# Kernel tuning notes

Hardware: AMD Instinct MI355X
Metric: run time of the kernel (lower is better)

The kernel has to match this reference:

```python
import jax, jax.numpy as jnp
import numpy as np
from jax import lax

D_MODEL = 512
D_STATE = 16
D_CONV = 4
EXPAND = 2
D_INNER = EXPAND * D_MODEL
DT_RANK = (D_MODEL + 15) // 16  # 32


def _mamba_dir(x, in_w, conv_w, conv_b, xproj_w, dt_w, dt_b, A_log, D, out_w):
    # x: (B, L, d_model)
    B, L, _ = x.shape
    xz = jnp.einsum('bld,ed->ble', x, in_w)          # (B, L, 2*d_inner)
    xi, z = jnp.split(xz, 2, axis=-1)                # each (B, L, d_inner)
    # causal depthwise conv over time
    xc = xi.transpose(0, 2, 1)                       # (B, d_inner, L)
    xc = lax.conv_general_dilated(
        xc, conv_w, window_strides=(1,), padding=[(D_CONV - 1, 0)],
        feature_group_count=D_INNER, dimension_numbers=('NCH', 'OIH', 'NCH'))
    xi = jax.nn.silu(xc + conv_b[None, :, None]).transpose(0, 2, 1)  # (B, L, d_inner)
    # input-dependent SSM params
    x_dbl = jnp.einsum('bld,ed->ble', xi, xproj_w)   # (B, L, dt_rank + 2*d_state)
    dt, Bc, Cc = jnp.split(x_dbl, [DT_RANK, DT_RANK + D_STATE], axis=-1)
    delta = jax.nn.softplus(jnp.einsum('blr,dr->bld', dt, dt_w) + dt_b)  # (B, L, d_inner)
    A = -jnp.exp(A_log)                              # (d_inner, d_state)
    deltaA = jnp.exp(delta[..., None] * A)           # (B, L, d_inner, d_state)
    dBx = delta[..., None] * Bc[:, :, None, :] * xi[..., None]  # (B, L, d_inner, d_state)

    def step(h, inputs):
        dA_t, dBx_t, C_t = inputs
        h = dA_t * h + dBx_t                         # (B, d_inner, d_state)
        y = jnp.einsum('bdn,bn->bd', h, C_t)
        return h, y

    h0 = jnp.zeros((B, D_INNER, D_STATE), dtype=x.dtype)
    _, ys = lax.scan(step, h0,
                     (deltaA.transpose(1, 0, 2, 3),
                      dBx.transpose(1, 0, 2, 3),
                      Cc.transpose(1, 0, 2)))
    y = ys.transpose(1, 0, 2)                        # (B, L, d_inner)
    y = y + xi * D
    y = y * jax.nn.silu(z)
    return jnp.einsum('ble,de->bld', y, out_w)       # (B, L, d_model)


def _forward(x, f_in_w, f_conv_w, f_conv_b, f_xproj_w, f_dt_w, f_dt_b, f_A_log, f_D, f_out_w,
             b_in_w, b_conv_w, b_conv_b, b_xproj_w, b_dt_w, b_dt_b, b_A_log, b_D, b_out_w,
             fusion_w, fusion_b, ln_g, ln_b):
    out_fwd = _mamba_dir(x, f_in_w, f_conv_w, f_conv_b, f_xproj_w, f_dt_w, f_dt_b, f_A_log, f_D, f_out_w)
    x_flip = jnp.flip(x, axis=1)
    out_bwd = _mamba_dir(x_flip, b_in_w, b_conv_w, b_conv_b, b_xproj_w, b_dt_w, b_dt_b, b_A_log, b_D, b_out_w)
    out_bwd = jnp.flip(out_bwd, axis=1)
    fused = jnp.concatenate([out_fwd, out_bwd], axis=-1)     # (B, L, 2*d_model)
    out = jnp.einsum('blf,df->bld', fused, fusion_w) + fusion_b
    r = x + out
    mu = jnp.mean(r, axis=-1, keepdims=True)
    var = jnp.var(r, axis=-1, keepdims=True)
    return (r - mu) * lax.rsqrt(var + 1e-5) * ln_g + ln_b


def _mamba_params(key):
    ks = jax.random.split(key, 6)
    s = 0.02
    in_w = jax.random.normal(ks[0], (2 * D_INNER, D_MODEL), jnp.float32) * s
    conv_w = jax.random.normal(ks[1], (D_INNER, 1, D_CONV), jnp.float32) * 0.2
    conv_b = jnp.zeros((D_INNER,), jnp.float32)
    xproj_w = jax.random.normal(ks[2], (DT_RANK + 2 * D_STATE, D_INNER), jnp.float32) * s
    dt_w = jax.random.normal(ks[3], (D_INNER, DT_RANK), jnp.float32) * (DT_RANK ** -0.5)
    dt_b = jax.random.uniform(ks[4], (D_INNER,), jnp.float32, -4.0, -2.0)
    A_log = jnp.log(jnp.broadcast_to(jnp.arange(1, D_STATE + 1, dtype=jnp.float32), (D_INNER, D_STATE)))
    D = jnp.ones((D_INNER,), jnp.float32)
    out_w = jax.random.normal(ks[5], (D_MODEL, D_INNER), jnp.float32) * s
    return in_w, conv_w, conv_b, xproj_w, dt_w, dt_b, A_log, D, out_w


def setup_inputs() -> dict:
    key = jax.random.key(0)
    kx, kf, kb, k1, k2 = jax.random.split(key, 5)
    B, L = 2, 1024
    x = jax.random.normal(kx, (B, L, D_MODEL), jnp.float32)
    f = _mamba_params(kf)
    b = _mamba_params(kb)
    fusion_w = jax.random.normal(k1, (D_MODEL, 2 * D_MODEL), jnp.float32) * 0.02
    fusion_b = jnp.zeros((D_MODEL,), jnp.float32)
    ln_g = jnp.ones((D_MODEL,), jnp.float32)
    ln_b = jnp.zeros((D_MODEL,), jnp.float32)
    names_f = ['f_in_w', 'f_conv_w', 'f_conv_b', 'f_xproj_w', 'f_dt_w', 'f_dt_b', 'f_A_log', 'f_D', 'f_out_w']
    names_b = ['b_in_w', 'b_conv_w', 'b_conv_b', 'b_xproj_w', 'b_dt_w', 'b_dt_b', 'b_A_log', 'b_D', 'b_out_w']
    d = {'x': x, 'fusion_w': fusion_w, 'fusion_b': fusion_b, 'ln_g': ln_g, 'ln_b': ln_b}
    d.update(dict(zip(names_f, f)))
    d.update(dict(zip(names_b, b)))
    return d


def reference(x, f_in_w, f_conv_w, f_conv_b, f_xproj_w, f_dt_w, f_dt_b, f_A_log, f_D, f_out_w,
              b_in_w, b_conv_w, b_conv_b, b_xproj_w, b_dt_w, b_dt_b, b_A_log, b_D, b_out_w,
              fusion_w, fusion_b, ln_g, ln_b):
    return _forward(x, f_in_w, f_conv_w, f_conv_b, f_xproj_w, f_dt_w, f_dt_b, f_A_log, f_D, f_out_w,
                    b_in_w, b_conv_w, b_conv_b, b_xproj_w, b_dt_w, b_dt_b, b_A_log, b_D, b_out_w,
                    fusion_w, fusion_b, ln_g, ln_b)
```

## Files before the change

kernel.cpp:

```cpp
#include <hip/hip_runtime.h>
#include <hip/hip_bf16.h>

typedef __bf16 bf16x8 __attribute__((ext_vector_type(8)));
typedef __bf16 bf16x4 __attribute__((ext_vector_type(4)));
typedef float  f32x4  __attribute__((ext_vector_type(4)));

#define LOG2E 1.44269504088896340f

static __device__ __forceinline__ unsigned short f2bf_bits(float f) {
  unsigned u = __builtin_bit_cast(unsigned, f);
  u = u + 0x7FFFu + ((u >> 16) & 1u);
  return (unsigned short)(u >> 16);
}
static __device__ __forceinline__ __bf16 to_bf16(float f) {
  unsigned short s = f2bf_bits(f);
  return __builtin_bit_cast(__bf16, s);
}
static __device__ __forceinline__ float fast_sigmoid(float x) {
  return __builtin_amdgcn_rcpf(1.f + __builtin_amdgcn_exp2f(-LOG2E * x));
}
static __device__ __forceinline__ float softplus_f(float x) {
  float m = fmaxf(x, 0.f);
  float e = __builtin_amdgcn_exp2f(-LOG2E * fabsf(x));
  return fmaf(__builtin_amdgcn_logf(1.f + e), 1.f / LOG2E, m);
}

struct CastSeg { const float* src; __bf16* dst; int n4; };
struct CastArgs { CastSeg s[8]; };

__global__ __launch_bounds__(256) void cast_kernel(CastArgs a) {
  CastSeg seg = a.s[blockIdx.y];
  int idx = blockIdx.x * 256 + threadIdx.x;
  int stride = gridDim.x * 256;
  const float4* src = (const float4*)seg.src;
  bf16x4* dst = (bf16x4*)seg.dst;
  for (int i = idx; i < seg.n4; i += stride) {
    float4 v = src[i];
    bf16x4 o;
    o[0] = to_bf16(v.x); o[1] = to_bf16(v.y);
    o[2] = to_bf16(v.z); o[3] = to_bf16(v.w);
    dst[i] = o;
  }
}

template<typename OutT, bool BIAS, bool RESID, bool SPLIT>
__global__ __launch_bounds__(256) void gemm_bt(
    const __bf16* __restrict__ A, long long sAz,
    const __bf16* __restrict__ B0, const __bf16* __restrict__ B1,
    OutT* __restrict__ C, long long sCz, int ldc,
    int N, int K,
    const float* __restrict__ bias, const float* __restrict__ resid, int ldr,
    float* __restrict__ xiout, __bf16* __restrict__ gateout, long long sXz)
{
  const __bf16* B = (blockIdx.z == 0) ? B0 : B1;
  A += (size_t)blockIdx.z * (size_t)sAz;
  C += (size_t)blockIdx.z * (size_t)sCz;
  if (SPLIT) {
    xiout  += (size_t)blockIdx.z * (size_t)sXz;
    gateout += (size_t)blockIdx.z * (size_t)sXz;
  }
  int lane = threadIdx.x & 63;
  int wid  = threadIdx.x >> 6;
  int rowBase = blockIdx.y * 128 + (wid >> 1) * 64;
  int colBase = blockIdx.x * 128 + (wid & 1) * 64;
  int lr = lane & 15;
  int lk = (lane >> 4) << 3;
  const __bf16* Ap = A + (size_t)(rowBase + lr) * K + lk;
  const __bf16* Bp[4];
  #pragma unroll
  for (int ni = 0; ni < 4; ++ni) {
    int br = colBase + ni * 16 + lr;
    if (br > N - 1) br = N - 1;
    Bp[ni] = B + (size_t)br * K + lk;
  }
  f32x4 acc[4][4] = {};
  #pragma unroll 2
  for (int k = 0; k < K; k += 32) {
    bf16x8 aF[4], bF[4];
    #pragma unroll
    for (int mi = 0; mi < 4; ++mi)
      aF[mi] = *(const bf16x8*)(Ap + (size_t)(mi * 16) * K + k);
    #pragma unroll
    for (int ni = 0; ni < 4; ++ni)
      bF[ni] = *(const bf16x8*)(Bp[ni] + k);
    #pragma unroll
    for (int mi = 0; mi < 4; ++mi)
      #pragma unroll
      for (int ni = 0; ni < 4; ++ni)
        acc[mi][ni] = __builtin_amdgcn_mfma_f32_16x16x32_bf16(aF[mi], bF[ni], acc[mi][ni], 0, 0, 0);
  }
  int crow = rowBase + ((lane >> 4) << 2);
  int ccol = colBase + lr;
  #pragma unroll
  for (int mi = 0; mi < 4; ++mi) {
    #pragma unroll
    for (int ni = 0; ni < 4; ++ni) {
      int c = ccol + ni * 16;
      if (c < N) {
        #pragma unroll
        for (int j = 0; j < 4; ++j) {
          int r = crow + mi * 16 + j;
          float v = acc[mi][ni][j];
          if (SPLIT) {
            if (c < 1024) xiout[(size_t)r * 1024 + c] = v;
            else          gateout[(size_t)r * 1024 + (c - 1024)] =
                              to_bf16(v * fast_sigmoid(v));
          } else {
            if (BIAS)  v += bias[c];
            if (RESID) v += resid[(size_t)r * ldr + c];
            if constexpr (sizeof(OutT) == 2) C[(size_t)r * ldc + c] = to_bf16(v);
            else                             C[(size_t)r * ldc + c] = v;
          }
        }
      }
    }
  }
}

#define CT 16
__global__ __launch_bounds__(256) void conv_silu_kernel(
    const float* __restrict__ xiraw,
    const float* __restrict__ f_cw, const float* __restrict__ f_cb,
    const float* __restrict__ b_cw, const float* __restrict__ b_cb,
    float* __restrict__ xi32,
    __bf16* __restrict__ xi16)
{
  int d  = blockIdx.x * 256 + threadIdx.x;
  int t0 = blockIdx.y * CT;
  int dir = blockIdx.z >> 1, b = blockIdx.z & 1;
  const float* cw = dir ? b_cw : f_cw;
  const float* cb = dir ? b_cb : f_cb;
  float w0 = cw[d*4+0], w1 = cw[d*4+1], w2 = cw[d*4+2], w3 = cw[d*4+3];
  float bias = cb[d];
  size_t rowBase = (size_t)dir * 2048 + (size_t)b * 1024;
  const float* xp = xiraw + rowBase * 1024 + d;
  float* o32 = xi32 + rowBase * 1024 + d;
  __bf16* o16 = xi16 + rowBase * 1024 + d;
  float xv[CT + 3];
  if (dir == 0) {
    #pragma unroll
    for (int j = 0; j < CT + 3; ++j) {
      int t = t0 - 3 + j;
      xv[j] = (t >= 0) ? xp[(size_t)t * 1024] : 0.f;
    }
    #pragma unroll
    for (int j = 0; j < CT; ++j) {
      int t = t0 + j;
      float v = fmaf(w0, xv[j], fmaf(w1, xv[j+1], fmaf(w2, xv[j+2], fmaf(w3, xv[j+3], bias))));
      float s = v * fast_sigmoid(v);
      o32[(size_t)t * 1024] = s;
      o16[(size_t)t * 1024] = to_bf16(s);
    }
  } else {
    #pragma unroll
    for (int j = 0; j < CT + 3; ++j) {
      int t = t0 + j;
      xv[j] = (t < 1024) ? xp[(size_t)t * 1024] : 0.f;
    }
    #pragma unroll
    for (int j = 0; j < CT; ++j) {
      int t = t0 + j;
      float v = fmaf(w3, xv[j], fmaf(w2, xv[j+1], fmaf(w1, xv[j+2], fmaf(w0, xv[j+3], bias))));
      float s = v * fast_sigmoid(v);
      o32[(size_t)t * 1024] = s;
      o16[(size_t)t * 1024] = to_bf16(s);
    }
  }
}

__global__ __launch_bounds__(256) void g2_kernel(
    const __bf16* __restrict__ A,
    const __bf16* __restrict__ B0, const __bf16* __restrict__ B1,
    float* __restrict__ partial)
{
  int slice = blockIdx.x;
  int mt = blockIdx.y;
  int dir = blockIdx.z;
  const __bf16* B = dir ? B1 : B0;
  const __bf16* Ad = A + (size_t)dir * 2048 * 1024;
  int lane = threadIdx.x & 63, wid = threadIdx.x >> 6;
  int rowBase = mt * 64 + wid * 16;
  int lr = lane & 15, lk = (lane >> 4) << 3;
  int k0 = slice * 256;
  const __bf16* Ap = Ad + (size_t)(rowBase + lr) * 1024 + k0 + lk;
  const __bf16* Bp[4];
  #pragma unroll
  for (int ni = 0; ni < 4; ++ni)
    Bp[ni] = B + (size_t)(ni * 16 + lr) * 1024 + k0 + lk;
  f32x4 acc[4] = {};
  #pragma unroll
  for (int k = 0; k < 256; k += 32) {
    bf16x8 aF = *(const bf16x8*)(Ap + k);
    #pragma unroll
    for (int ni = 0; ni < 4; ++ni) {
      bf16x8 bF = *(const bf16x8*)(Bp[ni] + k);
      acc[ni] = __builtin_amdgcn_mfma_f32_16x16x32_bf16(aF, bF, acc[ni], 0, 0, 0);
    }
  }
  int crow = rowBase + ((lane >> 4) << 2);
  float* out = partial + ((size_t)dir * 4 + slice) * 2048 * 64;
  #pragma unroll
  for (int ni = 0; ni < 4; ++ni)
    #pragma unroll
    for (int j = 0; j < 4; ++j)
      out[(size_t)(crow + j) * 64 + ni * 16 + lr] = acc[ni][j];
}

__global__ __launch_bounds__(256) void g2red_kernel(
    const float4* __restrict__ partial, float4* __restrict__ xdbl)
{
  int idx = blockIdx.x * 256 + threadIdx.x;
  int dir = idx >> 15;
  int rest = idx & 32767;
  const float4* p = partial + (size_t)dir * 4 * 32768 + rest;
  float4 a = p[0], b = p[32768], c = p[2 * 32768], d = p[3 * 32768];
  float4 s;
  s.x = a.x + b.x + c.x + d.x;
  s.y = a.y + b.y + c.y + d.y;
  s.z = a.z + b.z + c.z + d.z;
  s.w = a.w + b.w + c.w + d.w;
  xdbl[idx] = s;
}

#define NC 64
#define CL 16

__global__ __launch_bounds__(256) void scan_part1(
    const float* __restrict__ xi32,
    const float* __restrict__ xdbl,
    const float* __restrict__ f_dtw, const float* __restrict__ f_dtb,
    const float* __restrict__ b_dtw, const float* __restrict__ b_dtb,
    const float* __restrict__ f_Alog, const float* __restrict__ b_Alog,
    float4* __restrict__ aProd, float4* __restrict__ hPart)
{
  int d = blockIdx.x * 256 + threadIdx.x;
  int g = blockIdx.y;
  int zb = blockIdx.z;
  int dir = zb >> 1, b = zb & 1;
  const float* dtw = (dir ? b_dtw : f_dtw) + d * 32;
  float w[32];
  #pragma unroll
  for (int k = 0; k < 32; ++k) w[k] = dtw[k];
  float dtb = (dir ? b_dtb : f_dtb)[d];
  const float* Alog = (dir ? b_Alog : f_Alog) + d * 16;
  float As[16];
  #pragma unroll
  for (int n = 0; n < 16; ++n)
    As[n] = -__builtin_amdgcn_exp2f(LOG2E * Alog[n]) * LOG2E;
  int base = dir * 2048 + b * 1024;
  float h[16], A[16];
  #pragma unroll
  for (int n = 0; n < 16; ++n) { h[n] = 0.f; A[n] = 1.f; }
  #pragma unroll
  for (int j = 0; j < CL; ++j) {
    int tau = g * CL + j;
    int row = base + (dir ? (1023 - tau) : tau);
    const float* xr = xdbl + (size_t)row * 64;
    float acc = dtb;
    #pragma unroll
    for (int k = 0; k < 32; ++k) acc = fmaf(w[k], xr[k], acc);
    float del = softplus_f(acc);
    float xi = xi32[(size_t)row * 1024 + d];
    float dx = del * xi;
    #pragma unroll
    for (int n = 0; n < 16; ++n) {
      float dA = __builtin_amdgcn_exp2f(del * As[n]);
      h[n] = fmaf(dA, h[n], dx * xr[32 + n]);
      A[n] *= dA;
    }
  }
  size_t o = (((size_t)zb * NC + g) * 1024 + d) * 4;
  #pragma unroll
  for (int q = 0; q < 4; ++q) {
    aProd[o + q] = float4{A[q*4+0], A[q*4+1], A[q*4+2], A[q*4+3]};
    hPart[o + q] = float4{h[q*4+0], h[q*4+1], h[q*4+2], h[q*4+3]};
  }
}

__global__ __launch_bounds__(256) void scan_combine(
    const float* __restrict__ aProd, const float* __restrict__ hPart,
    float* __restrict__ hIn)
{
  int idx = blockIdx.x * 256 + threadIdx.x;
  int zb = idx >> 14;
  int dn = idx & 16383;
  float H = 0.f;
  #pragma unroll 8
  for (int g = 0; g < NC; ++g) {
    size_t o = ((size_t)zb * NC + g) * 16384 + dn;
    float a = aProd[o];
    float hp = hPart[o];
    hIn[o] = H;
    H = fmaf(a, H, hp);
  }
}

__global__ __launch_bounds__(256) void scan_part3(
    const float* __restrict__ xi32,
    const float* __restrict__ xdbl,
    const __bf16* __restrict__ gatebf,
    const float* __restrict__ f_dtw, const float* __restrict__ f_dtb,
    const float* __restrict__ b_dtw, const float* __restrict__ b_dtb,
    const float* __restrict__ f_Alog, const float* __restrict__ b_Alog,
    const float* __restrict__ f_D, const float* __restrict__ b_D,
    const float* __restrict__ hIn,
    __bf16* __restrict__ yout)
{
  int d = blockIdx.x * 256 + threadIdx.x;
  int g = blockIdx.y;
  int zb = blockIdx.z;
  int dir = zb >> 1, b = zb & 1;
  const float* dtw = (dir ? b_dtw : f_dtw) + d * 32;
  float w[32];
  #pragma unroll
  for (int k = 0; k < 32; ++k) w[k] = dtw[k];
  float dtb = (dir ? b_dtb : f_dtb)[d];
  float Dv = (dir ? b_D : f_D)[d];
  const float* Alog = (dir ? b_Alog : f_Alog) + d * 16;
  float As[16];
  #pragma unroll
  for (int n = 0; n < 16; ++n)
    As[n] = -__builtin_amdgcn_exp2f(LOG2E * Alog[n]) * LOG2E;
  float h[16];
  const float4* hi4 = (const float4*)(hIn + (((size_t)zb * NC + g) * 1024 + d) * 16);
  #pragma unroll
  for (int q = 0; q < 4; ++q) {
    float4 hv = hi4[q];
    h[q*4+0] = hv.x; h[q*4+1] = hv.y; h[q*4+2] = hv.z; h[q*4+3] = hv.w;
  }
  int base = dir * 2048 + b * 1024;
  #pragma unroll
  for (int j = 0; j < CL; ++j) {
    int tau = g * CL + j;
    int row = base + (dir ? (1023 - tau) : tau);
    const float* xr = xdbl + (size_t)row * 64;
    float acc = dtb;
    #pragma unroll
    for (int k = 0; k < 32; ++k) acc = fmaf(w[k], xr[k], acc);
    float del = softplus_f(acc);
    float xi = xi32[(size_t)row * 1024 + d];
    float dx = del * xi;
    float ps = 0.f;
    #pragma unroll
    for (int n = 0; n < 16; ++n) {
      float dA = __builtin_amdgcn_exp2f(del * As[n]);
      h[n] = fmaf(dA, h[n], dx * xr[32 + n]);
      ps = fmaf(h[n], xr[48 + n], ps);
    }
    float gate = (float)gatebf[(size_t)row * 1024 + d];
    float y = fmaf(xi, Dv, ps) * gate;
    yout[(size_t)row * 1024 + d] = to_bf16(y);
  }
}

__global__ __launch_bounds__(256) void ln_kernel(
    const float* __restrict__ r, const float* __restrict__ g,
    const float* __restrict__ beta, float* __restrict__ out)
{
  int row = blockIdx.x;
  int tid = threadIdx.x;
  const float* rp = r + (size_t)row * 512;
  float v0 = rp[tid], v1 = rp[tid + 256];
  float s = v0 + v1;
  float q = fmaf(v0, v0, v1 * v1);
  #pragma unroll
  for (int m = 1; m < 64; m <<= 1) {
    s += __shfl_xor(s, m, 64);
    q += __shfl_xor(q, m, 64);
  }
  __shared__ float ls[4], lq[4];
  int wid = tid >> 6;
  if ((tid & 63) == 0) { ls[wid] = s; lq[wid] = q; }
  __syncthreads();
  s = ls[0] + ls[1] + ls[2] + ls[3];
  q = lq[0] + lq[1] + lq[2] + lq[3];
  float mu = s * (1.f / 512.f);
  float var = q * (1.f / 512.f) - mu * mu;
  float rs = rsqrtf(var + 1e-5f);
  float* op = out + (size_t)row * 512;
  op[tid]       = (v0 - mu) * rs * g[tid]       + beta[tid];
  op[tid + 256] = (v1 - mu) * rs * g[tid + 256] + beta[tid + 256];
}

extern "C" void kernel_launch(void* const* d_in, const int* in_sizes, int n_in,
                              void* d_out, int out_size, void* d_ws, size_t ws_size,
                              hipStream_t stream)
{
  const float* x        = (const float*)d_in[0];
  const float* fusion_w = (const float*)d_in[1];
  const float* fusion_b = (const float*)d_in[2];
  const float* ln_g     = (const float*)d_in[3];
  const float* ln_b     = (const float*)d_in[4];
  const float* f_in_w   = (const float*)d_in[5];
  const float* f_conv_w = (const float*)d_in[6];
  const float* f_conv_b = (const float*)d_in[7];
  const float* f_xproj  = (const float*)d_in[8];
  const float* f_dt_w   = (const float*)d_in[9];
  const float* f_dt_b   = (const float*)d_in[10];
  const float* f_A_log  = (const float*)d_in[11];
  const float* f_D      = (const float*)d_in[12];
  const float* f_out_w  = (const float*)d_in[13];
  const float* b_in_w   = (const float*)d_in[14];
  const float* b_conv_w = (const float*)d_in[15];
  const float* b_conv_b = (const float*)d_in[16];
  const float* b_xproj  = (const float*)d_in[17];
  const float* b_dt_w   = (const float*)d_in[18];
  const float* b_dt_b   = (const float*)d_in[19];
  const float* b_A_log  = (const float*)d_in[20];
  const float* b_D      = (const float*)d_in[21];
  const float* b_out_w  = (const float*)d_in[22];

  char* w = (char*)d_ws;
  auto alloc = [&](size_t bytes) -> char* {
    char* p = w;
    w += (bytes + 255) & ~(size_t)255;
    return p;
  };
  __bf16* xbf    = (__bf16*)alloc((size_t)2048 * 512 * 2);
  __bf16* wInF   = (__bf16*)alloc((size_t)2048 * 512 * 2);
  __bf16* wInB   = (__bf16*)alloc((size_t)2048 * 512 * 2);
  __bf16* xprF   = (__bf16*)alloc((size_t)64 * 1024 * 2);
  __bf16* xprB   = (__bf16*)alloc((size_t)64 * 1024 * 2);
  __bf16* wOutF  = (__bf16*)alloc((size_t)512 * 1024 * 2);
  __bf16* wOutB  = (__bf16*)alloc((size_t)512 * 1024 * 2);
  __bf16* wFus   = (__bf16*)alloc((size_t)512 * 1024 * 2);
  float*  xiraw  = (float*)alloc((size_t)2 * 2048 * 1024 * 4);
  __bf16* gatebf = (__bf16*)alloc((size_t)2 * 2048 * 1024 * 2);
  float*  xi32   = (float*)alloc((size_t)2 * 2048 * 1024 * 4);
  __bf16* xi16   = (__bf16*)alloc((size_t)2 * 2048 * 1024 * 2);
  float*  part2  = (float*)alloc((size_t)2 * 4 * 2048 * 64 * 4);
  float*  xdbl   = (float*)alloc((size_t)2 * 2048 * 64 * 4);
  __bf16* ybf    = (__bf16*)alloc((size_t)2 * 2048 * 1024 * 2);
  __bf16* fin    = (__bf16*)alloc((size_t)2048 * 1024 * 2);
  float*  rbuf   = (float*)alloc((size_t)2048 * 512 * 4);
  float*  aProd  = (float*)alloc((size_t)4 * NC * 16384 * 4);
  float*  hPart  = (float*)alloc((size_t)4 * NC * 16384 * 4);
  float*  hInB   = (float*)alloc((size_t)4 * NC * 16384 * 4);
  (void)ws_size; (void)n_in; (void)in_sizes; (void)out_size;

  CastArgs ca;
  ca.s[0] = { x,        xbf,   (2048 * 512) / 4 };
  ca.s[1] = { f_in_w,   wInF,  (2048 * 512) / 4 };
  ca.s[2] = { b_in_w,   wInB,  (2048 * 512) / 4 };
  ca.s[3] = { f_xproj,  xprF,  (64 * 1024) / 4 };
  ca.s[4] = { b_xproj,  xprB,  (64 * 1024) / 4 };
  ca.s[5] = { f_out_w,  wOutF, (512 * 1024) / 4 };
  ca.s[6] = { b_out_w,  wOutB, (512 * 1024) / 4 };
  ca.s[7] = { fusion_w, wFus,  (512 * 1024) / 4 };
  cast_kernel<<<dim3(256, 8), 256, 0, stream>>>(ca);

  gemm_bt<float, false, false, true><<<dim3(16, 16, 2), 256, 0, stream>>>(
      xbf, 0LL, wInF, wInB, (float*)nullptr, 0LL, 0, 2048, 512,
      nullptr, nullptr, 0, xiraw, gatebf, (long long)2048 * 1024);

  conv_silu_kernel<<<dim3(4, 1024 / CT, 4), 256, 0, stream>>>(
      xiraw, f_conv_w, f_conv_b, b_conv_w, b_conv_b, xi32, xi16);

  g2_kernel<<<dim3(4, 32, 2), 256, 0, stream>>>(xi16, xprF, xprB, part2);
  g2red_kernel<<<dim3(256), 256, 0, stream>>>((const float4*)part2, (float4*)xdbl);

  scan_part1<<<dim3(4, NC, 4), 256, 0, stream>>>(
      xi32, xdbl, f_dt_w, f_dt_b, b_dt_w, b_dt_b, f_A_log, b_A_log,
      (float4*)aProd, (float4*)hPart);
  scan_combine<<<dim3(256), 256, 0, stream>>>(aProd, hPart, hInB);
  scan_part3<<<dim3(4, NC, 4), 256, 0, stream>>>(
      xi32, xdbl, gatebf, f_dt_w, f_dt_b, b_dt_w, b_dt_b, f_A_log, b_A_log,
      f_D, b_D, hInB, ybf);

  gemm_bt<__bf16, false, false, false><<<dim3(4, 16, 2), 256, 0, stream>>>(
      ybf, (long long)2048 * 1024, wOutF, wOutB, fin, 512LL, 1024, 512, 1024,
      nullptr, nullptr, 0, nullptr, nullptr, 0LL);

  gemm_bt<float, true, true, false><<<dim3(4, 16, 1), 256, 0, stream>>>(
      fin, 0LL, wFus, wFus, rbuf, 0LL, 512, 512, 1024,
      fusion_b, x, 512, nullptr, nullptr, 0LL);

  ln_kernel<<<2048, 256, 0, stream>>>(rbuf, ln_g, ln_b, (float*)d_out);
}
```

Before: 310.6 us.

## Store intermediates in bf16, precompute delta once, shrink GEMM row tiles

The pre-conv activation is now written in bf16 and the fp32 copy of the conv output is dropped, so the scan kernels read bf16 xi. The delta projection plus softplus moves into a new delta_kernel that writes bf16, where before both scan passes recomputed it. The output and fusion GEMMs use half-height row tiles to launch twice as many blocks. This cuts memory traffic and duplicated arithmetic, at the cost of lower precision in xi and delta and one extra launch.

```diff
diff --git a/kernel.cpp b/kernel.cpp
--- a/kernel.cpp
+++ b/kernel.cpp
@@ -43,25 +43,25 @@
   }
 }
 
-template<typename OutT, bool BIAS, bool RESID, bool SPLIT>
+template<typename OutT, bool BIAS, bool RESID, bool SPLIT, int MI>
 __global__ __launch_bounds__(256) void gemm_bt(
     const __bf16* __restrict__ A, long long sAz,
     const __bf16* __restrict__ B0, const __bf16* __restrict__ B1,
     OutT* __restrict__ C, long long sCz, int ldc,
     int N, int K,
     const float* __restrict__ bias, const float* __restrict__ resid, int ldr,
-    float* __restrict__ xiout, __bf16* __restrict__ gateout, long long sXz)
+    __bf16* __restrict__ xiout, __bf16* __restrict__ gateout, long long sXz)
 {
   const __bf16* B = (blockIdx.z == 0) ? B0 : B1;
   A += (size_t)blockIdx.z * (size_t)sAz;
   C += (size_t)blockIdx.z * (size_t)sCz;
   if (SPLIT) {
-    xiout  += (size_t)blockIdx.z * (size_t)sXz;
+    xiout   += (size_t)blockIdx.z * (size_t)sXz;
     gateout += (size_t)blockIdx.z * (size_t)sXz;
   }
   int lane = threadIdx.x & 63;
   int wid  = threadIdx.x >> 6;
-  int rowBase = blockIdx.y * 128 + (wid >> 1) * 64;
+  int rowBase = blockIdx.y * (MI * 32) + (wid >> 1) * (MI * 16);
   int colBase = blockIdx.x * 128 + (wid & 1) * 64;
   int lr = lane & 15;
   int lk = (lane >> 4) << 3;
@@ -73,18 +73,18 @@
     if (br > N - 1) br = N - 1;
     Bp[ni] = B + (size_t)br * K + lk;
   }
-  f32x4 acc[4][4] = {};
+  f32x4 acc[MI][4] = {};
   #pragma unroll 2
   for (int k = 0; k < K; k += 32) {
-    bf16x8 aF[4], bF[4];
-    #pragma unroll
-    for (int mi = 0; mi < 4; ++mi)
+    bf16x8 aF[MI], bF[4];
+    #pragma unroll
+    for (int mi = 0; mi < MI; ++mi)
       aF[mi] = *(const bf16x8*)(Ap + (size_t)(mi * 16) * K + k);
     #pragma unroll
     for (int ni = 0; ni < 4; ++ni)
       bF[ni] = *(const bf16x8*)(Bp[ni] + k);
     #pragma unroll
-    for (int mi = 0; mi < 4; ++mi)
+    for (int mi = 0; mi < MI; ++mi)
       #pragma unroll
       for (int ni = 0; ni < 4; ++ni)
         acc[mi][ni] = __builtin_amdgcn_mfma_f32_16x16x32_bf16(aF[mi], bF[ni], acc[mi][ni], 0, 0, 0);
@@ -92,7 +92,7 @@
   int crow = rowBase + ((lane >> 4) << 2);
   int ccol = colBase + lr;
   #pragma unroll
-  for (int mi = 0; mi < 4; ++mi) {
+  for (int mi = 0; mi < MI; ++mi) {
     #pragma unroll
     for (int ni = 0; ni < 4; ++ni) {
       int c = ccol + ni * 16;
@@ -102,7 +102,7 @@
           int r = crow + mi * 16 + j;
           float v = acc[mi][ni][j];
           if (SPLIT) {
-            if (c < 1024) xiout[(size_t)r * 1024 + c] = v;
+            if (c < 1024) xiout[(size_t)r * 1024 + c] = to_bf16(v);
             else          gateout[(size_t)r * 1024 + (c - 1024)] =
                               to_bf16(v * fast_sigmoid(v));
           } else {
@@ -119,10 +119,9 @@
 
 #define CT 16
 __global__ __launch_bounds__(256) void conv_silu_kernel(
-    const float* __restrict__ xiraw,
+    const __bf16* __restrict__ xiraw,
     const float* __restrict__ f_cw, const float* __restrict__ f_cb,
     const float* __restrict__ b_cw, const float* __restrict__ b_cb,
-    float* __restrict__ xi32,
     __bf16* __restrict__ xi16)
 {
   int d  = blockIdx.x * 256 + threadIdx.x;
@@ -133,36 +132,33 @@
   float w0 = cw[d*4+0], w1 = cw[d*4+1], w2 = cw[d*4+2], w3 = cw[d*4+3];
   float bias = cb[d];
   size_t rowBase = (size_t)dir * 2048 + (size_t)b * 1024;
-  const float* xp = xiraw + rowBase * 1024 + d;
-  float* o32 = xi32 + rowBase * 1024 + d;
+  const __bf16* xp = xiraw + rowBase * 1024 + d;
   __bf16* o16 = xi16 + rowBase * 1024 + d;
   float xv[CT + 3];
   if (dir == 0) {
     #pragma unroll
     for (int j = 0; j < CT + 3; ++j) {
       int t = t0 - 3 + j;
-      xv[j] = (t >= 0) ? xp[(size_t)t * 1024] : 0.f;
+      xv[j] = (t >= 0) ? (float)xp[(size_t)t * 1024] : 0.f;
     }
     #pragma unroll
     for (int j = 0; j < CT; ++j) {
       int t = t0 + j;
       float v = fmaf(w0, xv[j], fmaf(w1, xv[j+1], fmaf(w2, xv[j+2], fmaf(w3, xv[j+3], bias))));
       float s = v * fast_sigmoid(v);
-      o32[(size_t)t * 1024] = s;
       o16[(size_t)t * 1024] = to_bf16(s);
     }
   } else {
     #pragma unroll
     for (int j = 0; j < CT + 3; ++j) {
       int t = t0 + j;
-      xv[j] = (t < 1024) ? xp[(size_t)t * 1024] : 0.f;
+      xv[j] = (t < 1024) ? (float)xp[(size_t)t * 1024] : 0.f;
     }
     #pragma unroll
     for (int j = 0; j < CT; ++j) {
       int t = t0 + j;
       float v = fmaf(w3, xv[j], fmaf(w2, xv[j+1], fmaf(w1, xv[j+2], fmaf(w0, xv[j+3], bias))));
       float s = v * fast_sigmoid(v);
-      o32[(size_t)t * 1024] = s;
       o16[(size_t)t * 1024] = to_bf16(s);
     }
   }
@@ -222,14 +218,37 @@
   xdbl[idx] = s;
 }
 
-#define NC 64
-#define CL 16
-
-__global__ __launch_bounds__(256) void scan_part1(
-    const float* __restrict__ xi32,
+__global__ __launch_bounds__(256) void delta_kernel(
     const float* __restrict__ xdbl,
     const float* __restrict__ f_dtw, const float* __restrict__ f_dtb,
     const float* __restrict__ b_dtw, const float* __restrict__ b_dtb,
+    __bf16* __restrict__ delta16)
+{
+  int d = blockIdx.x * 256 + threadIdx.x;
+  int dir = blockIdx.z;
+  const float* dtw = (dir ? b_dtw : f_dtw) + d * 32;
+  float w[32];
+  #pragma unroll
+  for (int k = 0; k < 32; ++k) w[k] = dtw[k];
+  float dtb = (dir ? b_dtb : f_dtb)[d];
+  int row0 = dir * 2048 + blockIdx.y * 16;
+  #pragma unroll
+  for (int r = 0; r < 16; ++r) {
+    int row = row0 + r;
+    const float* xr = xdbl + (size_t)row * 64;
+    float acc = dtb;
+    #pragma unroll
+    for (int k = 0; k < 32; ++k) acc = fmaf(w[k], xr[k], acc);
+    delta16[(size_t)row * 1024 + d] = to_bf16(softplus_f(acc));
+  }
+}
+
+#define NC 64
+#define CL 16
+
+__global__ __launch_bounds__(256) void scan_part1(
+    const __bf16* __restrict__ delta16, const __bf16* __restrict__ xi16,
+    const float* __restrict__ xdbl,
     const float* __restrict__ f_Alog, const float* __restrict__ b_Alog,
     float4* __restrict__ aProd, float4* __restrict__ hPart)
 {
@@ -237,11 +256,6 @@
   int g = blockIdx.y;
   int zb = blockIdx.z;
   int dir = zb >> 1, b = zb & 1;
-  const float* dtw = (dir ? b_dtw : f_dtw) + d * 32;
-  float w[32];
-  #pragma unroll
-  for (int k = 0; k < 32; ++k) w[k] = dtw[k];
-  float dtb = (dir ? b_dtb : f_dtb)[d];
   const float* Alog = (dir ? b_Alog : f_Alog) + d * 16;
   float As[16];
   #pragma unroll
@@ -256,11 +270,8 @@
     int tau = g * CL + j;
     int row = base + (dir ? (1023 - tau) : tau);
     const float* xr = xdbl + (size_t)row * 64;
-    float acc = dtb;
-    #pragma unroll
-    for (int k = 0; k < 32; ++k) acc = fmaf(w[k], xr[k], acc);
-    float del = softplus_f(acc);
-    float xi = xi32[(size_t)row * 1024 + d];
+    float del = (float)delta16[(size_t)row * 1024 + d];
+    float xi  = (float)xi16[(size_t)row * 1024 + d];
     float dx = del * xi;
     #pragma unroll
     for (int n = 0; n < 16; ++n) {
@@ -296,11 +307,9 @@
 }
 
 __global__ __launch_bounds__(256) void scan_part3(
-    const float* __restrict__ xi32,
+    const __bf16* __restrict__ delta16, const __bf16* __restrict__ xi16,
     const float* __restrict__ xdbl,
     const __bf16* __restrict__ gatebf,
-    const float* __restrict__ f_dtw, const float* __restrict__ f_dtb,
-    const float* __restrict__ b_dtw, const float* __restrict__ b_dtb,
     const float* __restrict__ f_Alog, const float* __restrict__ b_Alog,
     const float* __restrict__ f_D, const float* __restrict__ b_D,
     const float* __restrict__ hIn,
@@ -310,11 +319,6 @@
   int g = blockIdx.y;
   int zb = blockIdx.z;
   int dir = zb >> 1, b = zb & 1;
-  const float* dtw = (dir ? b_dtw : f_dtw) + d * 32;
-  float w[32];
-  #pragma unroll
-  for (int k = 0; k < 32; ++k) w[k] = dtw[k];
-  float dtb = (dir ? b_dtb : f_dtb)[d];
   float Dv = (dir ? b_D : f_D)[d];
   const float* Alog = (dir ? b_Alog : f_Alog) + d * 16;
   float As[16];
@@ -334,11 +338,8 @@
     int tau = g * CL + j;
     int row = base + (dir ? (1023 - tau) : tau);
     const float* xr = xdbl + (size_t)row * 64;
-    float acc = dtb;
-    #pragma unroll
-    for (int k = 0; k < 32; ++k) acc = fmaf(w[k], xr[k], acc);
-    float del = softplus_f(acc);
-    float xi = xi32[(size_t)row * 1024 + d];
+    float del = (float)delta16[(size_t)row * 1024 + d];
+    float xi  = (float)xi16[(size_t)row * 1024 + d];
     float dx = del * xi;
     float ps = 0.f;
     #pragma unroll
@@ -424,12 +425,12 @@
   __bf16* wOutF  = (__bf16*)alloc((size_t)512 * 1024 * 2);
   __bf16* wOutB  = (__bf16*)alloc((size_t)512 * 1024 * 2);
   __bf16* wFus   = (__bf16*)alloc((size_t)512 * 1024 * 2);
-  float*  xiraw  = (float*)alloc((size_t)2 * 2048 * 1024 * 4);
+  __bf16* xiraw  = (__bf16*)alloc((size_t)2 * 2048 * 1024 * 2);
   __bf16* gatebf = (__bf16*)alloc((size_t)2 * 2048 * 1024 * 2);
-  float*  xi32   = (float*)alloc((size_t)2 * 2048 * 1024 * 4);
   __bf16* xi16   = (__bf16*)alloc((size_t)2 * 2048 * 1024 * 2);
   float*  part2  = (float*)alloc((size_t)2 * 4 * 2048 * 64 * 4);
   float*  xdbl   = (float*)alloc((size_t)2 * 2048 * 64 * 4);
+  __bf16* delta16= (__bf16*)alloc((size_t)2 * 2048 * 1024 * 2);
   __bf16* ybf    = (__bf16*)alloc((size_t)2 * 2048 * 1024 * 2);
   __bf16* fin    = (__bf16*)alloc((size_t)2048 * 1024 * 2);
   float*  rbuf   = (float*)alloc((size_t)2048 * 512 * 4);
@@ -449,29 +450,30 @@
   ca.s[7] = { fusion_w, wFus,  (512 * 1024) / 4 };
   cast_kernel<<<dim3(256, 8), 256, 0, stream>>>(ca);
 
-  gemm_bt<float, false, false, true><<<dim3(16, 16, 2), 256, 0, stream>>>(
+  gemm_bt<float, false, false, true, 4><<<dim3(16, 16, 2), 256, 0, stream>>>(
       xbf, 0LL, wInF, wInB, (float*)nullptr, 0LL, 0, 2048, 512,
       nullptr, nullptr, 0, xiraw, gatebf, (long long)2048 * 1024);
 
   conv_silu_kernel<<<dim3(4, 1024 / CT, 4), 256, 0, stream>>>(
-      xiraw, f_conv_w, f_conv_b, b_conv_w, b_conv_b, xi32, xi16);
+      xiraw, f_conv_w, f_conv_b, b_conv_w, b_conv_b, xi16);
 
   g2_kernel<<<dim3(4, 32, 2), 256, 0, stream>>>(xi16, xprF, xprB, part2);
   g2red_kernel<<<dim3(256), 256, 0, stream>>>((const float4*)part2, (float4*)xdbl);
 
+  delta_kernel<<<dim3(4, 128, 2), 256, 0, stream>>>(
+      xdbl, f_dt_w, f_dt_b, b_dt_w, b_dt_b, delta16);
+
   scan_part1<<<dim3(4, NC, 4), 256, 0, stream>>>(
-      xi32, xdbl, f_dt_w, f_dt_b, b_dt_w, b_dt_b, f_A_log, b_A_log,
-      (float4*)aProd, (float4*)hPart);
+      delta16, xi16, xdbl, f_A_log, b_A_log, (float4*)aProd, (float4*)hPart);
   scan_combine<<<dim3(256), 256, 0, stream>>>(aProd, hPart, hInB);
   scan_part3<<<dim3(4, NC, 4), 256, 0, stream>>>(
-      xi32, xdbl, gatebf, f_dt_w, f_dt_b, b_dt_w, b_dt_b, f_A_log, b_A_log,
-      f_D, b_D, hInB, ybf);
-
-  gemm_bt<__bf16, false, false, false><<<dim3(4, 16, 2), 256, 0, stream>>>(
+      delta16, xi16, xdbl, gatebf, f_A_log, b_A_log, f_D, b_D, hInB, ybf);
+
+  gemm_bt<__bf16, false, false, false, 2><<<dim3(4, 32, 2), 256, 0, stream>>>(
       ybf, (long long)2048 * 1024, wOutF, wOutB, fin, 512LL, 1024, 512, 1024,
       nullptr, nullptr, 0, nullptr, nullptr, 0LL);
 
-  gemm_bt<float, true, true, false><<<dim3(4, 16, 1), 256, 0, stream>>>(
+  gemm_bt<float, true, true, false, 2><<<dim3(4, 32, 1), 256, 0, stream>>>(
       fin, 0LL, wFus, wFus, rbuf, 0LL, 512, 512, 1024,
       fusion_b, x, 512, nullptr, nullptr, 0LL);
 
```

Result: faster. 282.5 us (-9.0%).
